# Kernel tuning notes

Hardware: AMD Instinct MI355X
Metric: run time of the kernel (lower is better)

## Reference

```python
import jax, jax.numpy as jnp
import numpy as np

E, T, H, I, K = 8, 4096, 1024, 2048, 2
N_LAYER = 24
STD = 0.02


def setup_inputs() -> dict:
    key = jax.random.key(0)
    k1, k2, k3, k4, k5 = jax.random.split(key, 5)
    hidden_states = jax.random.normal(k1, (T, H), dtype=jnp.float32)
    rw = jax.random.uniform(k2, (T, K), dtype=jnp.float32)
    routing_weights = rw / rw.sum(-1, keepdims=True)  # top-k gates sum to 1
    selected_experts = jax.random.randint(k3, (T, K), 0, E)
    w_fc = jax.random.normal(k4, (E, H, I), dtype=jnp.float32) * STD
    w_proj = jax.random.normal(k5, (E, I, H), dtype=jnp.float32) * (STD / np.sqrt(2.0 * N_LAYER))
    return {
        "hidden_states": hidden_states,
        "routing_weights": routing_weights,
        "selected_experts": selected_experts,
        "w_fc": w_fc,
        "w_proj": w_proj,
    }


def reference(hidden_states, routing_weights, selected_experts, w_fc, w_proj):
    # hidden_states: [T, H]; routing_weights/selected_experts: [T, K]
    # w_fc: [E, H, I]; w_proj: [E, I, H]
    n_tokens = hidden_states.shape[0]
    n_experts = w_fc.shape[0]
    # Per-token total gate mass per expert (duplicate expert picks sum): [T, E]
    gates = jnp.zeros((n_tokens, n_experts), dtype=hidden_states.dtype)
    gates = gates.at[jnp.arange(n_tokens)[:, None], selected_experts].add(routing_weights)
    # Equivalent to scatter-dispatch grouped GEMM: each (token, k) pair routed to
    # expert e yields gate * (gelu(x @ Wfc[e]) @ Wproj[e]); identical pairs sum.
    out = jnp.zeros_like(hidden_states)
    for e in range(n_experts):  # small fixed expert count
        h = jax.nn.gelu(hidden_states @ w_fc[e], approximate=False)  # [T, I]
        y = h @ w_proj[e]  # [T, H]
        out = out + gates[:, e:e + 1] * y
    return out
```

## Files before the change

kernel.cpp:

```cpp
#include <hip/hip_runtime.h>
#include <cstdint>
#include <cstddef>

#define E_EXPERTS 8
#define T_TOKENS  4096
#define HDIM      1024
#define IDIM      2048
#define TOPK      2
#define NPAIR     (T_TOKENS * TOPK)

#define BM 128
#define BN 128
#define BK 32

#define MAX_SLOTS 9216
#define MAX_TILES 72

#define M_NTILES 0
#define M_TOTAL  1
#define M_TE     8
#define M_TS     (8 + MAX_TILES)

#define OFF_TOK  4096
#define OFF_GATE (OFF_TOK + MAX_SLOTS * 4)
#define OFF_XG   81920
#define OFF_H    (OFF_XG + (size_t)MAX_SLOTS * HDIM * 2)
#define OFF_WT   (OFF_H  + (size_t)MAX_SLOTS * IDIM * 2)
#define WS_NEED  (OFF_WT + (size_t)E_EXPERTS * HDIM * IDIM * 2)

typedef __bf16 bf16x8 __attribute__((ext_vector_type(8)));
typedef float  f32x4  __attribute__((ext_vector_type(4)));

__device__ __forceinline__ unsigned short f2bf(float x) {
    union { float f; unsigned u; } v; v.f = x;
    unsigned r = v.u + 0x7fff + ((v.u >> 16) & 1);
    return (unsigned short)(r >> 16);
}

__global__ void k_route(const float* __restrict__ rw, const int* __restrict__ sel,
                        int* __restrict__ meta, int* __restrict__ slot_token,
                        float* __restrict__ slot_gate) {
    __shared__ int cnt[E_EXPERTS];
    __shared__ int cur[E_EXPERTS];
    __shared__ int off[E_EXPERTS + 1];
    const int tid = threadIdx.x;
    if (tid < E_EXPERTS) cnt[tid] = 0;
    __syncthreads();
    for (int i = tid; i < NPAIR; i += blockDim.x) atomicAdd(&cnt[sel[i]], 1);
    __syncthreads();
    if (tid == 0) {
        int o = 0, t = 0;
        for (int e = 0; e < E_EXPERTS; ++e) {
            off[e] = o; cur[e] = o;
            int nt = (cnt[e] + BM - 1) / BM;
            for (int i = 0; i < nt; ++i) { meta[M_TE + t] = e; meta[M_TS + t] = o + i * BM; ++t; }
            o += nt * BM;
        }
        off[E_EXPERTS] = o;
        meta[M_NTILES] = t;
        meta[M_TOTAL]  = o;
    }
    __syncthreads();
    const int total = off[E_EXPERTS];
    for (int s = tid; s < total; s += blockDim.x) { slot_token[s] = -1; slot_gate[s] = 0.f; }
    __syncthreads();
    for (int i = tid; i < NPAIR; i += blockDim.x) {
        int e = sel[i];
        int pos = atomicAdd(&cur[e], 1);
        slot_token[pos] = i >> 1;
        slot_gate[pos]  = rw[i];
    }
}

__global__ void k_transpose_cvt(const float* __restrict__ W, unsigned short* __restrict__ WT,
                                int R, int C) {
    __shared__ unsigned short tile[32][33];
    const int e  = blockIdx.z;
    const int c0 = blockIdx.x * 32, r0 = blockIdx.y * 32;
    const float* src = W + (size_t)e * R * C;
    unsigned short* dst = WT + (size_t)e * R * C;
    #pragma unroll
    for (int i = threadIdx.y; i < 32; i += 8)
        tile[i][threadIdx.x] = f2bf(src[(size_t)(r0 + i) * C + c0 + threadIdx.x]);
    __syncthreads();
    #pragma unroll
    for (int i = threadIdx.y; i < 32; i += 8)
        dst[(size_t)(c0 + i) * R + r0 + threadIdx.x] = tile[threadIdx.x][i];
}

__global__ void k_gather(const float* __restrict__ hidden, const int* __restrict__ meta,
                         const int* __restrict__ slot_token, unsigned short* __restrict__ Xg) {
    const int s = blockIdx.x;
    if (s >= meta[M_TOTAL]) return;
    const int tok = slot_token[s];
    const int tid = threadIdx.x;
    ushort4 o4;
    if (tok >= 0) {
        const float4 v = *(const float4*)(hidden + (size_t)tok * HDIM + tid * 4);
        o4.x = f2bf(v.x); o4.y = f2bf(v.y); o4.z = f2bf(v.z); o4.w = f2bf(v.w);
    } else {
        o4 = make_ushort4(0, 0, 0, 0);
    }
    *(ushort4*)(Xg + (size_t)s * HDIM + tid * 4) = o4;
}

template <int NTOT, int KTOT, bool FUSE_GELU>
__global__ __launch_bounds__(256, 2) void k_moe_gemm(
    const unsigned short* __restrict__ A, const unsigned short* __restrict__ Bw,
    unsigned short* __restrict__ Hout,
    const int* __restrict__ slot_token, const float* __restrict__ slot_gate,
    float* __restrict__ out, const int* __restrict__ meta)
{
    const int t = blockIdx.x;
    if (t >= meta[M_NTILES]) return;
    const int e     = meta[M_TE + t];
    const int slot0 = meta[M_TS + t];
    const int bn0   = blockIdx.y * BN;

    __shared__ __align__(16) char lds[2 * 16384];

    const int tid  = threadIdx.x;
    const int lane = tid & 63;
    const int wave = tid >> 6;
    const int wr = wave >> 1, wc = wave & 1;

    const unsigned short* Abase = A  + (size_t)slot0 * KTOT;
    const unsigned short* Bbase = Bw + ((size_t)e * NTOT + bn0) * KTOT;

    auto stage = [&](int buf, int kt) {
        const int k0 = kt * BK;
        #pragma unroll
        for (int r = 0; r < 2; ++r) {
            int o    = tid * 16 + r * 4096;
            int row  = o >> 6;
            int colb = o & 63;
            int scolb = colb ^ ((row & 3) << 4);
            int ge = k0 + (scolb >> 1);
            __builtin_amdgcn_global_load_lds(
                (const __attribute__((address_space(1))) void*)(Abase + (size_t)row * KTOT + ge),
                (__attribute__((address_space(3))) void*)(lds + buf * 16384 + o), 16, 0, 0);
            __builtin_amdgcn_global_load_lds(
                (const __attribute__((address_space(1))) void*)(Bbase + (size_t)row * KTOT + ge),
                (__attribute__((address_space(3))) void*)(lds + buf * 16384 + 8192 + o), 16, 0, 0);
        }
    };

    f32x4 acc[4][4] = {};

    stage(0, 0);
    asm volatile("s_waitcnt vmcnt(0)" ::: "memory");
    __syncthreads();

    const int nk = KTOT / BK;
    const int lk = (lane >> 4) * 16;
    int cur = 0;
    for (int kt = 0; kt < nk; ++kt) {
        if (kt + 1 < nk) stage(cur ^ 1, kt + 1);
        const char* Al = lds + cur * 16384;
        const char* Bl = Al + 8192;
        bf16x8 af[4], bfr[4];
        #pragma unroll
        for (int m = 0; m < 4; ++m) {
            int row = wr * 64 + m * 16 + (lane & 15);
            af[m] = *(const bf16x8*)(Al + row * 64 + (lk ^ ((row & 3) << 4)));
        }
        #pragma unroll
        for (int n = 0; n < 4; ++n) {
            int row = wc * 64 + n * 16 + (lane & 15);
            bfr[n] = *(const bf16x8*)(Bl + row * 64 + (lk ^ ((row & 3) << 4)));
        }
        #pragma unroll
        for (int m = 0; m < 4; ++m)
            #pragma unroll
            for (int n = 0; n < 4; ++n)
                acc[m][n] = __builtin_amdgcn_mfma_f32_16x16x32_bf16(af[m], bfr[n], acc[m][n], 0, 0, 0);
        asm volatile("s_waitcnt vmcnt(0)" ::: "memory");
        __syncthreads();
        cur ^= 1;
    }

    if constexpr (FUSE_GELU) {
        #pragma unroll
        for (int m = 0; m < 4; ++m)
            #pragma unroll
            for (int n = 0; n < 4; ++n) {
                const int colabs = bn0 + wc * 64 + n * 16 + (lane & 15);
                #pragma unroll
                for (int j = 0; j < 4; ++j) {
                    const int rowrel = wr * 64 + m * 16 + ((lane >> 4) << 2) + j;
                    float x = acc[m][n][j];
                    float g = 0.5f * x * (1.0f + erff(x * 0.70710678118654752f));
                    Hout[(size_t)(slot0 + rowrel) * NTOT + colabs] = f2bf(g);
                }
            }
    } else {
        #pragma unroll
        for (int m = 0; m < 4; ++m) {
            int tok[4]; float gt[4];
            #pragma unroll
            for (int j = 0; j < 4; ++j) {
                const int rs = slot0 + wr * 64 + m * 16 + ((lane >> 4) << 2) + j;
                tok[j] = slot_token[rs];
                gt[j]  = slot_gate[rs];
            }
            #pragma unroll
            for (int n = 0; n < 4; ++n) {
                const int colabs = bn0 + wc * 64 + n * 16 + (lane & 15);
                #pragma unroll
                for (int j = 0; j < 4; ++j)
                    if (tok[j] >= 0)
                        atomicAdd(out + (size_t)tok[j] * NTOT + colabs, gt[j] * acc[m][n][j]);
            }
        }
    }
}

__global__ void k_sentinel(float* out, float v) { out[0] = v; }

extern "C" void kernel_launch(void* const* d_in, const int* in_sizes, int n_in,
                              void* d_out, int out_size, void* d_ws, size_t ws_size,
                              hipStream_t stream) {
    const float* hidden = (const float*)d_in[0];
    const float* rw     = (const float*)d_in[1];
    const int*   sel    = (const int*)  d_in[2];
    const float* w_fc   = (const float*)d_in[3];
    const float* w_proj = (const float*)d_in[4];
    float* out = (float*)d_out;
    char*  ws  = (char*)d_ws;

    if (ws_size < WS_NEED) {
        k_sentinel<<<1, 1, 0, stream>>>(out, (float)ws_size);
        return;
    }

    int*            meta       = (int*)ws;
    int*            slot_token = (int*)(ws + OFF_TOK);
    float*          slot_gate  = (float*)(ws + OFF_GATE);
    unsigned short* Xg         = (unsigned short*)(ws + OFF_XG);
    unsigned short* Hbuf       = (unsigned short*)(ws + OFF_H);
    unsigned short* WT         = (unsigned short*)(ws + OFF_WT);

    hipMemsetAsync(d_out, 0, (size_t)out_size * sizeof(float), stream);

    k_route<<<1, 1024, 0, stream>>>(rw, sel, meta, slot_token, slot_gate);

    k_transpose_cvt<<<dim3(IDIM / 32, HDIM / 32, E_EXPERTS), dim3(32, 8), 0, stream>>>(
        w_fc, WT, HDIM, IDIM);

    k_gather<<<MAX_SLOTS, 256, 0, stream>>>(hidden, meta, slot_token, Xg);

    k_moe_gemm<IDIM, HDIM, true><<<dim3(MAX_TILES, IDIM / BN), 256, 0, stream>>>(
        Xg, WT, Hbuf, nullptr, nullptr, nullptr, meta);

    k_transpose_cvt<<<dim3(HDIM / 32, IDIM / 32, E_EXPERTS), dim3(32, 8), 0, stream>>>(
        w_proj, WT, IDIM, HDIM);

    k_moe_gemm<HDIM, IDIM, false><<<dim3(MAX_TILES, HDIM / BN), 256, 0, stream>>>(
        Hbuf, WT, nullptr, slot_token, slot_gate, out, meta);
}
```

Baseline: 376.4 us.

## Replace atomic scatter with combine kernel, triple-buffer GEMM, widen transpose, swizzle grid

The second GEMM no longer does float atomicAdd into the output. It writes gate-scaled bf16 rows into a slot buffer, and a new combine kernel sums each token's two slots through an inverse map built in routing. The GEMM K-loop moves to a three-stage LDS pipeline with partial vmcnt waits, a changed LDS swizzle and a flattened, XCD-interleaved block index. Routing uses wave-ballot aggregated atomics, and the weight transpose uses 64x64 tiles with vectorized loads and stores. The combine drops the output memset and atomic contention, but the down-projection result is now rounded to bf16 before the sum, and LDS use per block grows.

```diff
diff --git a/kernel.cpp b/kernel.cpp
--- a/kernel.cpp
+++ b/kernel.cpp
@@ -23,7 +23,8 @@
 
 #define OFF_TOK  4096
 #define OFF_GATE (OFF_TOK + MAX_SLOTS * 4)
-#define OFF_XG   81920
+#define OFF_INV  (OFF_GATE + MAX_SLOTS * 4)
+#define OFF_XG   131072
 #define OFF_H    (OFF_XG + (size_t)MAX_SLOTS * HDIM * 2)
 #define OFF_WT   (OFF_H  + (size_t)MAX_SLOTS * IDIM * 2)
 #define WS_NEED  (OFF_WT + (size_t)E_EXPERTS * HDIM * IDIM * 2)
@@ -36,56 +37,96 @@
     unsigned r = v.u + 0x7fff + ((v.u >> 16) & 1);
     return (unsigned short)(r >> 16);
 }
+__device__ __forceinline__ float bf2f(unsigned short b) {
+    union { unsigned u; float f; } v; v.u = ((unsigned)b) << 16; return v.f;
+}
 
 __global__ void k_route(const float* __restrict__ rw, const int* __restrict__ sel,
                         int* __restrict__ meta, int* __restrict__ slot_token,
-                        float* __restrict__ slot_gate) {
+                        float* __restrict__ slot_gate, int* __restrict__ inv) {
     __shared__ int cnt[E_EXPERTS];
     __shared__ int cur[E_EXPERTS];
-    __shared__ int off[E_EXPERTS + 1];
-    const int tid = threadIdx.x;
+    __shared__ int total_sh;
+    const int tid  = threadIdx.x;
+    const int lane = tid & 63;
+    const unsigned long long lt = (lane == 63) ? 0x7fffffffffffffffULL : ((1ULL << lane) - 1ULL);
     if (tid < E_EXPERTS) cnt[tid] = 0;
     __syncthreads();
-    for (int i = tid; i < NPAIR; i += blockDim.x) atomicAdd(&cnt[sel[i]], 1);
+    for (int i = tid; i < NPAIR; i += 1024) {
+        int e = sel[i];
+        #pragma unroll
+        for (int ex = 0; ex < E_EXPERTS; ++ex) {
+            unsigned long long m = __ballot(e == ex);
+            if (m && lane == (int)__builtin_ctzll(m))
+                atomicAdd(&cnt[ex], __popcll(m));
+        }
+    }
     __syncthreads();
     if (tid == 0) {
         int o = 0, t = 0;
         for (int e = 0; e < E_EXPERTS; ++e) {
-            off[e] = o; cur[e] = o;
+            cur[e] = o;
             int nt = (cnt[e] + BM - 1) / BM;
             for (int i = 0; i < nt; ++i) { meta[M_TE + t] = e; meta[M_TS + t] = o + i * BM; ++t; }
             o += nt * BM;
         }
-        off[E_EXPERTS] = o;
         meta[M_NTILES] = t;
         meta[M_TOTAL]  = o;
-    }
-    __syncthreads();
-    const int total = off[E_EXPERTS];
-    for (int s = tid; s < total; s += blockDim.x) { slot_token[s] = -1; slot_gate[s] = 0.f; }
-    __syncthreads();
-    for (int i = tid; i < NPAIR; i += blockDim.x) {
+        total_sh = o;
+    }
+    __syncthreads();
+    const int total = total_sh;
+    for (int s = tid; s < total; s += 1024) { slot_token[s] = -1; slot_gate[s] = 0.f; }
+    __syncthreads();
+    for (int i = tid; i < NPAIR; i += 1024) {
         int e = sel[i];
-        int pos = atomicAdd(&cur[e], 1);
+        float g = rw[i];
+        int pos = 0;
+        #pragma unroll
+        for (int ex = 0; ex < E_EXPERTS; ++ex) {
+            unsigned long long m = __ballot(e == ex);
+            if (m) {
+                int leader = (int)__builtin_ctzll(m);
+                int c = __popcll(m);
+                int base = 0;
+                if (lane == leader) base = atomicAdd(&cur[ex], c);
+                base = __shfl(base, leader);
+                if (e == ex) pos = base + __popcll(m & lt);
+            }
+        }
         slot_token[pos] = i >> 1;
-        slot_gate[pos]  = rw[i];
+        slot_gate[pos]  = g;
+        inv[i]          = pos;
     }
 }
 
 __global__ void k_transpose_cvt(const float* __restrict__ W, unsigned short* __restrict__ WT,
                                 int R, int C) {
-    __shared__ unsigned short tile[32][33];
+    __shared__ unsigned short tile[64][66];
     const int e  = blockIdx.z;
-    const int c0 = blockIdx.x * 32, r0 = blockIdx.y * 32;
+    const int c0 = blockIdx.x * 64, r0 = blockIdx.y * 64;
     const float* src = W + (size_t)e * R * C;
     unsigned short* dst = WT + (size_t)e * R * C;
+    const int tx = threadIdx.x, ty = threadIdx.y;
     #pragma unroll
-    for (int i = threadIdx.y; i < 32; i += 8)
-        tile[i][threadIdx.x] = f2bf(src[(size_t)(r0 + i) * C + c0 + threadIdx.x]);
+    for (int k = 0; k < 4; ++k) {
+        const float4 v = *(const float4*)(src + (size_t)(r0 + ty * 4 + k) * C + c0 + tx * 4);
+        tile[ty * 4 + k][tx * 4 + 0] = f2bf(v.x);
+        tile[ty * 4 + k][tx * 4 + 1] = f2bf(v.y);
+        tile[ty * 4 + k][tx * 4 + 2] = f2bf(v.z);
+        tile[ty * 4 + k][tx * 4 + 3] = f2bf(v.w);
+    }
     __syncthreads();
     #pragma unroll
-    for (int i = threadIdx.y; i < 32; i += 8)
-        dst[(size_t)(c0 + i) * R + r0 + threadIdx.x] = tile[threadIdx.x][i];
+    for (int k = 0; k < 4; ++k) {
+        const int c = c0 + ty * 4 + k;
+        ushort4 u;
+        u.x = tile[tx * 4 + 0][ty * 4 + k];
+        u.y = tile[tx * 4 + 1][ty * 4 + k];
+        u.z = tile[tx * 4 + 2][ty * 4 + k];
+        u.w = tile[tx * 4 + 3][ty * 4 + k];
+        *(ushort4*)(dst + (size_t)c * R + r0 + tx * 4) = u;
+    }
 }
 
 __global__ void k_gather(const float* __restrict__ hidden, const int* __restrict__ meta,
@@ -108,16 +149,19 @@
 __global__ __launch_bounds__(256, 2) void k_moe_gemm(
     const unsigned short* __restrict__ A, const unsigned short* __restrict__ Bw,
     unsigned short* __restrict__ Hout,
-    const int* __restrict__ slot_token, const float* __restrict__ slot_gate,
-    float* __restrict__ out, const int* __restrict__ meta)
+    const float* __restrict__ slot_gate, const int* __restrict__ meta)
 {
-    const int t = blockIdx.x;
+    constexpr int NBN = NTOT / BN;
+    const int nwg = MAX_TILES * NBN;
+    const int bid = blockIdx.x;
+    const int wg  = (bid & 7) * (nwg >> 3) + (bid >> 3);
+    const int t   = wg / NBN;
+    const int bn0 = (wg % NBN) * BN;
     if (t >= meta[M_NTILES]) return;
     const int e     = meta[M_TE + t];
     const int slot0 = meta[M_TS + t];
-    const int bn0   = blockIdx.y * BN;
-
-    __shared__ __align__(16) char lds[2 * 16384];
+
+    __shared__ __align__(16) char lds[3 * 16384];
 
     const int tid  = threadIdx.x;
     const int lane = tid & 63;
@@ -131,11 +175,11 @@
         const int k0 = kt * BK;
         #pragma unroll
         for (int r = 0; r < 2; ++r) {
-            int o    = tid * 16 + r * 4096;
-            int row  = o >> 6;
-            int colb = o & 63;
-            int scolb = colb ^ ((row & 3) << 4);
-            int ge = k0 + (scolb >> 1);
+            const int o   = tid * 16 + r * 4096;
+            const int row = o >> 6;
+            const int s   = (o & 63) >> 4;
+            const int q   = s ^ ((row >> 1) & 3);
+            const int ge  = k0 + q * 8;
             __builtin_amdgcn_global_load_lds(
                 (const __attribute__((address_space(1))) void*)(Abase + (size_t)row * KTOT + ge),
                 (__attribute__((address_space(3))) void*)(lds + buf * 16384 + o), 16, 0, 0);
@@ -146,38 +190,45 @@
     };
 
     f32x4 acc[4][4] = {};
-
-    stage(0, 0);
-    asm volatile("s_waitcnt vmcnt(0)" ::: "memory");
-    __syncthreads();
-
-    const int nk = KTOT / BK;
-    const int lk = (lane >> 4) * 16;
-    int cur = 0;
-    for (int kt = 0; kt < nk; ++kt) {
-        if (kt + 1 < nk) stage(cur ^ 1, kt + 1);
-        const char* Al = lds + cur * 16384;
+    const int lkq = (lane >> 4);
+
+    auto compute = [&](int buf) {
+        const char* Al = lds + buf * 16384;
         const char* Bl = Al + 8192;
         bf16x8 af[4], bfr[4];
         #pragma unroll
         for (int m = 0; m < 4; ++m) {
-            int row = wr * 64 + m * 16 + (lane & 15);
-            af[m] = *(const bf16x8*)(Al + row * 64 + (lk ^ ((row & 3) << 4)));
+            const int row = wr * 64 + m * 16 + (lane & 15);
+            af[m] = *(const bf16x8*)(Al + row * 64 + ((lkq ^ ((row >> 1) & 3)) << 4));
         }
         #pragma unroll
         for (int n = 0; n < 4; ++n) {
-            int row = wc * 64 + n * 16 + (lane & 15);
-            bfr[n] = *(const bf16x8*)(Bl + row * 64 + (lk ^ ((row & 3) << 4)));
+            const int row = wc * 64 + n * 16 + (lane & 15);
+            bfr[n] = *(const bf16x8*)(Bl + row * 64 + ((lkq ^ ((row >> 1) & 3)) << 4));
         }
         #pragma unroll
         for (int m = 0; m < 4; ++m)
             #pragma unroll
             for (int n = 0; n < 4; ++n)
                 acc[m][n] = __builtin_amdgcn_mfma_f32_16x16x32_bf16(af[m], bfr[n], acc[m][n], 0, 0, 0);
-        asm volatile("s_waitcnt vmcnt(0)" ::: "memory");
-        __syncthreads();
-        cur ^= 1;
-    }
+    };
+
+    const int nk = KTOT / BK;
+    stage(0, 0);
+    stage(1, 1);
+    asm volatile("s_waitcnt vmcnt(4)" ::: "memory");
+    __builtin_amdgcn_s_barrier();
+
+    for (int kt = 0; kt < nk - 2; ++kt) {
+        stage((kt + 2) % 3, kt + 2);
+        compute(kt % 3);
+        asm volatile("s_waitcnt vmcnt(4)" ::: "memory");
+        __builtin_amdgcn_s_barrier();
+    }
+    compute((nk - 2) % 3);
+    asm volatile("s_waitcnt vmcnt(0)" ::: "memory");
+    __builtin_amdgcn_s_barrier();
+    compute((nk - 1) % 3);
 
     if constexpr (FUSE_GELU) {
         #pragma unroll
@@ -188,31 +239,44 @@
                 #pragma unroll
                 for (int j = 0; j < 4; ++j) {
                     const int rowrel = wr * 64 + m * 16 + ((lane >> 4) << 2) + j;
-                    float x = acc[m][n][j];
-                    float g = 0.5f * x * (1.0f + erff(x * 0.70710678118654752f));
+                    const float x = acc[m][n][j];
+                    const float g = 0.5f * x * (1.0f + erff(x * 0.70710678118654752f));
                     Hout[(size_t)(slot0 + rowrel) * NTOT + colabs] = f2bf(g);
                 }
             }
     } else {
         #pragma unroll
         for (int m = 0; m < 4; ++m) {
-            int tok[4]; float gt[4];
+            float gt[4];
             #pragma unroll
-            for (int j = 0; j < 4; ++j) {
-                const int rs = slot0 + wr * 64 + m * 16 + ((lane >> 4) << 2) + j;
-                tok[j] = slot_token[rs];
-                gt[j]  = slot_gate[rs];
-            }
+            for (int j = 0; j < 4; ++j)
+                gt[j] = slot_gate[slot0 + wr * 64 + m * 16 + ((lane >> 4) << 2) + j];
             #pragma unroll
             for (int n = 0; n < 4; ++n) {
                 const int colabs = bn0 + wc * 64 + n * 16 + (lane & 15);
                 #pragma unroll
-                for (int j = 0; j < 4; ++j)
-                    if (tok[j] >= 0)
-                        atomicAdd(out + (size_t)tok[j] * NTOT + colabs, gt[j] * acc[m][n][j]);
+                for (int j = 0; j < 4; ++j) {
+                    const int rowrel = wr * 64 + m * 16 + ((lane >> 4) << 2) + j;
+                    Hout[(size_t)(slot0 + rowrel) * NTOT + colabs] = f2bf(gt[j] * acc[m][n][j]);
+                }
             }
         }
     }
+}
+
+__global__ void k_combine(const unsigned short* __restrict__ y, const int* __restrict__ inv,
+                          float* __restrict__ out) {
+    const int tk  = blockIdx.x;
+    const int tid = threadIdx.x;
+    const int p0 = inv[2 * tk], p1 = inv[2 * tk + 1];
+    const ushort4 a = ((const ushort4*)(y + (size_t)p0 * HDIM))[tid];
+    const ushort4 b = ((const ushort4*)(y + (size_t)p1 * HDIM))[tid];
+    float4 o;
+    o.x = bf2f(a.x) + bf2f(b.x);
+    o.y = bf2f(a.y) + bf2f(b.y);
+    o.z = bf2f(a.z) + bf2f(b.z);
+    o.w = bf2f(a.w) + bf2f(b.w);
+    ((float4*)(out + (size_t)tk * HDIM))[tid] = o;
 }
 
 __global__ void k_sentinel(float* out, float v) { out[0] = v; }
@@ -236,25 +300,26 @@
     int*            meta       = (int*)ws;
     int*            slot_token = (int*)(ws + OFF_TOK);
     float*          slot_gate  = (float*)(ws + OFF_GATE);
+    int*            inv        = (int*)(ws + OFF_INV);
     unsigned short* Xg         = (unsigned short*)(ws + OFF_XG);
     unsigned short* Hbuf       = (unsigned short*)(ws + OFF_H);
     unsigned short* WT         = (unsigned short*)(ws + OFF_WT);
 
-    hipMemsetAsync(d_out, 0, (size_t)out_size * sizeof(float), stream);
-
-    k_route<<<1, 1024, 0, stream>>>(rw, sel, meta, slot_token, slot_gate);
-
-    k_transpose_cvt<<<dim3(IDIM / 32, HDIM / 32, E_EXPERTS), dim3(32, 8), 0, stream>>>(
+    k_route<<<1, 1024, 0, stream>>>(rw, sel, meta, slot_token, slot_gate, inv);
+
+    k_transpose_cvt<<<dim3(IDIM / 64, HDIM / 64, E_EXPERTS), dim3(16, 16), 0, stream>>>(
         w_fc, WT, HDIM, IDIM);
 
     k_gather<<<MAX_SLOTS, 256, 0, stream>>>(hidden, meta, slot_token, Xg);
 
-    k_moe_gemm<IDIM, HDIM, true><<<dim3(MAX_TILES, IDIM / BN), 256, 0, stream>>>(
-        Xg, WT, Hbuf, nullptr, nullptr, nullptr, meta);
-
-    k_transpose_cvt<<<dim3(HDIM / 32, IDIM / 32, E_EXPERTS), dim3(32, 8), 0, stream>>>(
+    k_moe_gemm<IDIM, HDIM, true><<<MAX_TILES * (IDIM / BN), 256, 0, stream>>>(
+        Xg, WT, Hbuf, nullptr, meta);
+
+    k_transpose_cvt<<<dim3(HDIM / 64, IDIM / 64, E_EXPERTS), dim3(16, 16), 0, stream>>>(
         w_proj, WT, IDIM, HDIM);
 
-    k_moe_gemm<HDIM, IDIM, false><<<dim3(MAX_TILES, HDIM / BN), 256, 0, stream>>>(
-        Hbuf, WT, nullptr, slot_token, slot_gate, out, meta);
-}
+    k_moe_gemm<HDIM, IDIM, false><<<MAX_TILES * (HDIM / BN), 256, 0, stream>>>(
+        Hbuf, WT, Xg, slot_gate, meta);
+
+    k_combine<<<T_TOKENS, 256, 0, stream>>>(Xg, inv, out);
+}
```

New measurement: 327.9 us. 12.9% less time.
